# Performance work log

Hardware: AMD Instinct MI355X
Metric: run time of the kernel (lower is better)

Reference implementation:

```python
import jax, jax.numpy as jnp
import numpy as np
from jax import lax

B, H, W, CIN = 16, 96, 320, 32
N_ACTIVE = 200000
COUT = 256
FC_IN = (H // 8) * (W // 8) * 128  # 12*40*128 = 61440


def _conv(x, w, b):
    # stride-2, pad-1, 3x3 conv in NCHW / OIHW layout
    y = lax.conv_general_dilated(x, w, (2, 2), [(1, 1), (1, 1)],
                                 dimension_numbers=('NCHW', 'OIHW', 'NCHW'))
    return y + b[None, :, None, None]


def _maxpool3(x):
    # 3x3 maxpool, stride 1, pad 1 (NCHW)
    return lax.reduce_window(x, -jnp.inf, lax.max,
                             (1, 1, 3, 3), (1, 1, 1, 1),
                             [(0, 0), (0, 0), (1, 1), (1, 1)])


def setup_inputs() -> dict:
    key = jax.random.key(0)
    ks = jax.random.split(key, 12)
    input_feat = jax.random.normal(ks[0], (B, H, W, CIN), dtype=jnp.float32)
    cb = jax.random.randint(ks[1], (N_ACTIVE, 1), 0, B)
    cy = jax.random.randint(ks[2], (N_ACTIVE, 1), 0, H)
    cx = jax.random.randint(ks[3], (N_ACTIVE, 1), 0, W)
    spconv_coords = jnp.concatenate([cb, cy, cx], axis=1).astype(jnp.int32)
    w1 = jax.random.normal(ks[4], (32, CIN, 3, 3), dtype=jnp.float32) * (1.0 / np.sqrt(CIN * 9))
    b1 = jax.random.normal(ks[5], (32,), dtype=jnp.float32) * 0.01
    w2 = jax.random.normal(ks[6], (64, 32, 3, 3), dtype=jnp.float32) * (1.0 / np.sqrt(32 * 9))
    b2 = jax.random.normal(ks[7], (64,), dtype=jnp.float32) * 0.01
    w3 = jax.random.normal(ks[8], (128, 64, 3, 3), dtype=jnp.float32) * (1.0 / np.sqrt(64 * 9))
    b3 = jax.random.normal(ks[9], (128,), dtype=jnp.float32) * 0.01
    fc_w = jax.random.normal(ks[10], (COUT, FC_IN), dtype=jnp.float32) * (1.0 / np.sqrt(FC_IN))
    fc_b = jax.random.normal(ks[11], (COUT,), dtype=jnp.float32) * 0.01
    return {"input_feat": input_feat, "spconv_coords": spconv_coords,
            "w1": w1, "b1": b1, "w2": w2, "b2": b2, "w3": w3, "b3": b3,
            "fc_w": fc_w, "fc_b": fc_b}


def reference(input_feat, spconv_coords, w1, b1, w2, b2, w3, b3, fc_w, fc_b):
    bi = spconv_coords[:, 0]
    yi = spconv_coords[:, 1]
    xi = spconv_coords[:, 2]
    # gather active-site features, then scatter into a dense NHWC grid
    feats = input_feat[bi, yi, xi]                       # [N, CIN]
    dense = jnp.zeros_like(input_feat).at[bi, yi, xi].set(feats)
    x = dense.transpose(0, 3, 1, 2)                      # [B, CIN, H, W]
    x = jax.nn.relu(_maxpool3(_conv(x, w1, b1)))         # [B, 32, H/2, W/2]
    x = jax.nn.relu(_maxpool3(_conv(x, w2, b2)))         # [B, 64, H/4, W/4]
    x = jax.nn.relu(_maxpool3(_conv(x, w3, b3)))         # [B, 128, H/8, W/8]
    x = x.reshape(x.shape[0], -1)                        # [B, FC_IN]
    return jax.nn.relu(x @ fc_w.T + fc_b)                # [B, COUT]
```

## Files before the change

### kernel.cpp

```cpp
#include <hip/hip_runtime.h>

#define NB 16
#define NH 96
#define NW 320
#define NCIN 32

typedef __attribute__((ext_vector_type(8))) short short8;
typedef __attribute__((ext_vector_type(4))) float f32x4;

__device__ inline unsigned short f2bf(float f) {
    union { float f; unsigned int u; } v; v.f = f;
    unsigned int r = v.u + 0x7FFF + ((v.u >> 16) & 1);
    return (unsigned short)(r >> 16);
}

__global__ __launch_bounds__(256) void setup_all(const float* __restrict__ w1,
                                                 const float* __restrict__ w2,
                                                 const float* __restrict__ w3,
                                                 unsigned short* __restrict__ f1,
                                                 unsigned short* __restrict__ f2,
                                                 unsigned short* __restrict__ f3,
                                                 const int* __restrict__ coords,
                                                 const float* __restrict__ input,
                                                 unsigned short* __restrict__ inBf,
                                                 int n) {
    if (blockIdx.x < 396) {
        int i = blockIdx.x * 256 + threadIdx.x;
        if (i < 9216) {
            int j = i & 7, lane = (i >> 3) & 63, nt = (i >> 9) & 1, tap = i >> 10;
            int ic = ((lane >> 4) * 8) + j, oc = nt * 16 + (lane & 15);
            f1[i] = f2bf(w1[(oc * 32 + ic) * 9 + tap]);
        } else if (i < 27648) {
            int v = i - 9216;
            int j = v & 7, lane = (v >> 3) & 63, nt = (v >> 9) & 3, tap = v >> 11;
            int ic = ((lane >> 4) * 8) + j, oc = nt * 16 + (lane & 15);
            f2[v] = f2bf(w2[(oc * 32 + ic) * 9 + tap]);
        } else if (i < 101376) {
            int v = i - 27648;
            int j = v & 7, lane = (v >> 3) & 63, nt = (v >> 9) & 7, kk = v >> 12;
            int tap = kk >> 1, ks = kk & 1;
            int ic = ks * 32 + ((lane >> 4) * 8) + j, oc = nt * 16 + (lane & 15);
            f3[v] = f2bf(w3[(oc * 64 + ic) * 9 + tap]);
        }
    } else {
        int i = (blockIdx.x - 396) * 256 + threadIdx.x;
        if (i >= n * 4) return;
        int ci = i >> 2, q = i & 3;
        int b = coords[ci * 3 + 0], y = coords[ci * 3 + 1], x = coords[ci * 3 + 2];
        long base = ((long)((b * NH + y) * NW + x)) * NCIN + q * 8;
        const float4* src = (const float4*)(input + base);
        float4 v0 = src[0], v1 = src[1];
        union { short8 s8; unsigned short us[8]; } o;
        o.us[0] = f2bf(v0.x); o.us[1] = f2bf(v0.y); o.us[2] = f2bf(v0.z); o.us[3] = f2bf(v0.w);
        o.us[4] = f2bf(v1.x); o.us[5] = f2bf(v1.y); o.us[6] = f2bf(v1.z); o.us[7] = f2bf(v1.w);
        *(short8*)(inBf + base) = o.s8;
    }
}

template<int IC, int OC, int NL, int IH, int IW, int OH, int OW>
__global__ __launch_bounds__(256) void conv_mfma(
    const unsigned short* __restrict__ inPtr,
    const unsigned short* __restrict__ wfrag,
    const float* __restrict__ bias,
    float* __restrict__ out)
{
    constexpr int KS = IC / 32;
    constexpr int NT = OC / 16;
    constexpr int NG = NT / NL;
    constexpr int NSTRIPS = NB * OH * OW / 16;

    const int wid  = (blockIdx.x * 256 + threadIdx.x) >> 6;
    const int lane = threadIdx.x & 63;
    const int ntb  = (wid % NG) * NL;
    const int s    = wid / NG;
    if (s >= NSTRIPS) return;
    const int quad = lane >> 4;
    const int lm   = lane & 15;

    const int p0 = s * 16;
    const int posA = p0 + lm;
    const int b  = posA / (OH * OW);
    const int rr = posA % (OH * OW);
    const int oy = rr / OW, ox = rr % OW;
    const int iy0 = oy * 2 - 1, ix0 = ox * 2 - 1;

    int cell[9];
    bool okb[9];
    #pragma unroll
    for (int t9 = 0; t9 < 9; t9++) {
        const int iy = iy0 + t9 / 3;
        const int ix = ix0 + t9 % 3;
        const bool ok = (iy >= 0) && (iy < IH) && (ix >= 0) && (ix < IW);
        cell[t9] = ok ? ((b * IH + iy) * IW + ix) : 0;
        okb[t9] = ok;
    }

    short8 zero8;
    #pragma unroll
    for (int j = 0; j < 8; j++) zero8[j] = 0;

    f32x4 acc[NL][2];
    #pragma unroll
    for (int nl = 0; nl < NL; nl++)
        #pragma unroll
        for (int pp = 0; pp < 2; pp++)
            acc[nl][pp] = (f32x4){0.f, 0.f, 0.f, 0.f};

    #pragma unroll 1
    for (int ks = 0; ks < KS; ks++) {
        short8 av[9];
        #pragma unroll
        for (int t9 = 0; t9 < 9; t9++) {
            short8 v = *(const short8*)(inPtr + (long)cell[t9] * IC + ks * 32 + quad * 8);
            av[t9] = okb[t9] ? v : zero8;
        }
        #pragma unroll
        for (int nl = 0; nl < NL; nl++) {
            #pragma unroll
            for (int t9 = 0; t9 < 9; t9++) {
                short8 bf = *(const short8*)(wfrag + (((t9 * KS + ks) * NT + ntb + nl) * 64 + lane) * 8);
                if (t9 & 1) acc[nl][1] = __builtin_amdgcn_mfma_f32_16x16x32_bf16(av[t9], bf, acc[nl][1], 0, 0, 0);
                else        acc[nl][0] = __builtin_amdgcn_mfma_f32_16x16x32_bf16(av[t9], bf, acc[nl][0], 0, 0, 0);
            }
        }
    }

    const long rowBase = (long)p0 + quad * 4;
    #pragma unroll
    for (int nl = 0; nl < NL; nl++) {
        const int oc = (ntb + nl) * 16 + lm;
        const float bv = bias[oc];
        #pragma unroll
        for (int reg = 0; reg < 4; reg++)
            out[(rowBase + reg) * OC + oc] = acc[nl][0][reg] + acc[nl][1][reg] + bv;
    }
}

template<int C, int HH, int WW, bool BF16OUT>
__global__ __launch_bounds__(256) void maxpool3_relu(const float* __restrict__ in, void* __restrict__ outv) {
    constexpr int C4 = C / 4;
    int i = blockIdx.x * blockDim.x + threadIdx.x;
    if (i >= NB * HH * WW * C4) return;
    int c = i % C4;
    int x = (i / C4) % WW;
    int y = (i / (C4 * WW)) % HH;
    int b = i / (C4 * WW * HH);
    float4 m = make_float4(-3.0e38f, -3.0e38f, -3.0e38f, -3.0e38f);
    #pragma unroll
    for (int dy = -1; dy <= 1; dy++) {
        int yy = y + dy;
        if (yy < 0 || yy >= HH) continue;
        #pragma unroll
        for (int dx = -1; dx <= 1; dx++) {
            int xx = x + dx;
            if (xx < 0 || xx >= WW) continue;
            float4 v = ((const float4*)in)[((b * HH + yy) * WW + xx) * C4 + c];
            m.x = fmaxf(m.x, v.x);
            m.y = fmaxf(m.y, v.y);
            m.z = fmaxf(m.z, v.z);
            m.w = fmaxf(m.w, v.w);
        }
    }
    m.x = fmaxf(m.x, 0.f);
    m.y = fmaxf(m.y, 0.f);
    m.z = fmaxf(m.z, 0.f);
    m.w = fmaxf(m.w, 0.f);
    if (BF16OUT) {
        ushort4 o;
        o.x = f2bf(m.x); o.y = f2bf(m.y); o.z = f2bf(m.z); o.w = f2bf(m.w);
        ((ushort4*)outv)[i] = o;
    } else {
        ((float4*)outv)[i] = m;
    }
}

__global__ __launch_bounds__(256) void transpose_fc(const float* __restrict__ in, float* __restrict__ xT) {
    __shared__ float tile_s[32 * 16 * 17];
    const int pt = blockIdx.x % 30;
    const int ct = blockIdx.x / 30;
    const int pos0 = pt * 16, c0 = ct * 32;
    const int t = threadIdx.x;
    {
        const int b = t / 16, pl = t % 16;
        const float4* src = (const float4*)(in + ((long)(b * 480 + pos0 + pl)) * 128 + c0);
        #pragma unroll
        for (int q = 0; q < 8; q++) {
            float4 v = src[q];
            tile_s[((4 * q + 0) * 16 + pl) * 17 + b] = v.x;
            tile_s[((4 * q + 1) * 16 + pl) * 17 + b] = v.y;
            tile_s[((4 * q + 2) * 16 + pl) * 17 + b] = v.z;
            tile_s[((4 * q + 3) * 16 + pl) * 17 + b] = v.w;
        }
    }
    __syncthreads();
    {
        const int w = t / 64, l = t % 64;
        const int pl2 = l / 4, b4 = l % 4;
        #pragma unroll
        for (int i = 0; i < 8; i++) {
            int cl = w + 4 * i;
            const float* ls = &tile_s[(cl * 16 + pl2) * 17 + 4 * b4];
            float4 v = make_float4(ls[0], ls[1], ls[2], ls[3]);
            *(float4*)(xT + ((long)(c0 + cl) * 480 + pos0 + pl2) * 16 + 4 * b4) = v;
        }
    }
}

__global__ __launch_bounds__(256) void fc_stage1(const float* __restrict__ xT,
                                                 const float* __restrict__ fw,
                                                 float* __restrict__ partial)
{
    __shared__ float red[32 * 257];
    const int tile  = blockIdx.x / 15;
    const int chunk = blockIdx.x % 15;
    const int t = threadIdx.x;
    const int K = 61440, KC = 4096;

    float acc[4][16];
    #pragma unroll
    for (int o = 0; o < 4; o++)
        #pragma unroll
        for (int bb = 0; bb < 16; bb++) acc[o][bb] = 0.f;

    const int k0 = chunk * KC;
    #pragma unroll 2
    for (int k = k0 + t; k < k0 + KC; k += 256) {
        const float4* xp = (const float4*)(xT + (long)k * 16);
        float4 x0 = xp[0], x1 = xp[1], x2 = xp[2], x3 = xp[3];
        #pragma unroll
        for (int o = 0; o < 4; o++) {
            float w = fw[(long)(tile * 4 + o) * K + k];
            acc[o][0]  = fmaf(w, x0.x, acc[o][0]);
            acc[o][1]  = fmaf(w, x0.y, acc[o][1]);
            acc[o][2]  = fmaf(w, x0.z, acc[o][2]);
            acc[o][3]  = fmaf(w, x0.w, acc[o][3]);
            acc[o][4]  = fmaf(w, x1.x, acc[o][4]);
            acc[o][5]  = fmaf(w, x1.y, acc[o][5]);
            acc[o][6]  = fmaf(w, x1.z, acc[o][6]);
            acc[o][7]  = fmaf(w, x1.w, acc[o][7]);
            acc[o][8]  = fmaf(w, x2.x, acc[o][8]);
            acc[o][9]  = fmaf(w, x2.y, acc[o][9]);
            acc[o][10] = fmaf(w, x2.z, acc[o][10]);
            acc[o][11] = fmaf(w, x2.w, acc[o][11]);
            acc[o][12] = fmaf(w, x3.x, acc[o][12]);
            acc[o][13] = fmaf(w, x3.y, acc[o][13]);
            acc[o][14] = fmaf(w, x3.z, acc[o][14]);
            acc[o][15] = fmaf(w, x3.w, acc[o][15]);
        }
    }

    #pragma unroll
    for (int oo = 0; oo < 2; oo++)
        #pragma unroll
        for (int bb = 0; bb < 16; bb++)
            red[(oo * 16 + bb) * 257 + t] = acc[oo][bb];
    __syncthreads();
    if (t < 32) {
        float s = 0.f;
        for (int i = 0; i < 256; i++) s += red[t * 257 + i];
        partial[((long)chunk * 256 + tile * 4 + (t / 16)) * 16 + (t % 16)] = s;
    }
    __syncthreads();
    #pragma unroll
    for (int oo = 0; oo < 2; oo++)
        #pragma unroll
        for (int bb = 0; bb < 16; bb++)
            red[(oo * 16 + bb) * 257 + t] = acc[2 + oo][bb];
    __syncthreads();
    if (t < 32) {
        float s = 0.f;
        for (int i = 0; i < 256; i++) s += red[t * 257 + i];
        partial[((long)chunk * 256 + tile * 4 + 2 + (t / 16)) * 16 + (t % 16)] = s;
    }
}

__global__ __launch_bounds__(256) void fc_reduce(const float* __restrict__ partial,
                                                 const float* __restrict__ fcb,
                                                 float* __restrict__ out)
{
    int i = blockIdx.x * blockDim.x + threadIdx.x;
    if (i >= 4096) return;
    int oc = i / 16, b = i % 16;
    float s = fcb[oc];
    #pragma unroll
    for (int c = 0; c < 15; c++) s += partial[(c * 256 + oc) * 16 + b];
    out[b * 256 + oc] = fmaxf(s, 0.f);
}

extern "C" void kernel_launch(void* const* d_in, const int* in_sizes, int n_in,
                              void* d_out, int out_size, void* d_ws, size_t ws_size,
                              hipStream_t stream) {
    const float* input  = (const float*)d_in[0];
    const int*   coords = (const int*)d_in[1];
    const float* w1 = (const float*)d_in[2];
    const float* b1 = (const float*)d_in[3];
    const float* w2 = (const float*)d_in[4];
    const float* b2 = (const float*)d_in[5];
    const float* w3 = (const float*)d_in[6];
    const float* b3 = (const float*)d_in[7];
    const float* fcw = (const float*)d_in[8];
    const float* fcb = (const float*)d_in[9];
    float* outp = (float*)d_out;

    const int n_active = in_sizes[1] / 3;

    char* ws = (char*)d_ws;
    unsigned short* wf1 = (unsigned short*)ws;
    unsigned short* wf2 = wf1 + 9216;
    unsigned short* wf3 = wf2 + 18432;
    unsigned short* inBf = (unsigned short*)(ws + 204800);
    char* regA = ws + 204800 + 31457280;
    char* regB = regA + 15728640;
    float* partial = (float*)(regB + 7864320);

    float*          conv1o  = (float*)regA;
    unsigned short* pool1bf = (unsigned short*)regB;
    float*          conv2o  = (float*)regA;
    unsigned short* pool2bf = (unsigned short*)regB;
    float*          conv3o  = (float*)regA;
    float*          pool3f  = (float*)regB;
    float*          xT      = (float*)regA;

    hipMemsetAsync(inBf, 0, 31457280, stream);
    const int scatterBlocks = (n_active * 4 + 255) / 256;
    setup_all<<<396 + scatterBlocks, 256, 0, stream>>>(w1, w2, w3, wf1, wf2, wf3,
                                                       coords, input, inBf, n_active);

    conv_mfma<32, 32, 2, 96, 320, 48, 160>
        <<<1920, 256, 0, stream>>>(inBf, wf1, b1, conv1o);
    maxpool3_relu<32, 48, 160, true><<<3840, 256, 0, stream>>>(conv1o, pool1bf);

    conv_mfma<32, 64, 2, 48, 160, 24, 80>
        <<<960, 256, 0, stream>>>(pool1bf, wf2, b2, conv2o);
    maxpool3_relu<64, 24, 80, true><<<1920, 256, 0, stream>>>(conv2o, pool2bf);

    conv_mfma<64, 128, 2, 24, 80, 12, 40>
        <<<480, 256, 0, stream>>>(pool2bf, wf3, b3, conv3o);
    maxpool3_relu<128, 12, 40, false><<<960, 256, 0, stream>>>(conv3o, pool3f);

    transpose_fc<<<120, 256, 0, stream>>>(pool3f, xT);
    fc_stage1<<<960, 256, 0, stream>>>(xT, fcw, partial);
    fc_reduce<<<16, 256, 0, stream>>>(partial, fcb, outp);
}
```

Before: 246.8 us.

## Compute FC layer with bf16 MFMA and split-K across 240 chunks

Replaces the scalar FMA FC kernel with a wave-level bf16 MFMA kernel: each wave handles 16 output channels over a 256-wide K chunk, converting fp32 weights to bf16 on the fly. The transpose kernel now writes activations as bf16 in batch-major [B, K] layout to feed the MFMA A operand. The final reduction now sums 240 partials per output instead of 15. The aim is to cut FMA issue cost and the shared-memory reduction, at the cost of bf16 precision in the FC and more partial-sum traffic.

```diff
diff --git a/kernel.cpp b/kernel.cpp
--- a/kernel.cpp
+++ b/kernel.cpp
@@ -174,7 +174,8 @@
     }
 }
 
-__global__ __launch_bounds__(256) void transpose_fc(const float* __restrict__ in, float* __restrict__ xT) {
+__global__ __launch_bounds__(256) void transpose_fc(const float* __restrict__ in,
+                                                    unsigned short* __restrict__ xb) {
     __shared__ float tile_s[32 * 16 * 17];
     const int pt = blockIdx.x % 30;
     const int ct = blockIdx.x / 30;
@@ -194,83 +195,61 @@
     }
     __syncthreads();
     {
-        const int w = t / 64, l = t % 64;
-        const int pl2 = l / 4, b4 = l % 4;
-        #pragma unroll
-        for (int i = 0; i < 8; i++) {
-            int cl = w + 4 * i;
-            const float* ls = &tile_s[(cl * 16 + pl2) * 17 + 4 * b4];
-            float4 v = make_float4(ls[0], ls[1], ls[2], ls[3]);
-            *(float4*)(xT + ((long)(c0 + cl) * 480 + pos0 + pl2) * 16 + 4 * b4) = v;
-        }
-    }
-}
-
-__global__ __launch_bounds__(256) void fc_stage1(const float* __restrict__ xT,
-                                                 const float* __restrict__ fw,
-                                                 float* __restrict__ partial)
+        #pragma unroll
+        for (int r = 0; r < 2; r++) {
+            int seg = t * 2 + r;
+            int b = seg / 32, cl = seg % 32;
+            union { short8 s8; unsigned short us[8]; } o0, o1;
+            #pragma unroll
+            for (int pl = 0; pl < 8; pl++)
+                o0.us[pl] = f2bf(tile_s[(cl * 16 + pl) * 17 + b]);
+            #pragma unroll
+            for (int pl = 0; pl < 8; pl++)
+                o1.us[pl] = f2bf(tile_s[(cl * 16 + 8 + pl) * 17 + b]);
+            unsigned short* dst = xb + (long)b * 61440 + (c0 + cl) * 480 + pos0;
+            *(short8*)dst = o0.s8;
+            *(short8*)(dst + 8) = o1.s8;
+        }
+    }
+}
+
+__global__ __launch_bounds__(256) void fc_mfma(const unsigned short* __restrict__ xb,
+                                               const float* __restrict__ fw,
+                                               float* __restrict__ partial)
 {
-    __shared__ float red[32 * 257];
-    const int tile  = blockIdx.x / 15;
-    const int chunk = blockIdx.x % 15;
-    const int t = threadIdx.x;
-    const int K = 61440, KC = 4096;
-
-    float acc[4][16];
-    #pragma unroll
-    for (int o = 0; o < 4; o++)
-        #pragma unroll
-        for (int bb = 0; bb < 16; bb++) acc[o][bb] = 0.f;
-
-    const int k0 = chunk * KC;
-    #pragma unroll 2
-    for (int k = k0 + t; k < k0 + KC; k += 256) {
-        const float4* xp = (const float4*)(xT + (long)k * 16);
-        float4 x0 = xp[0], x1 = xp[1], x2 = xp[2], x3 = xp[3];
-        #pragma unroll
-        for (int o = 0; o < 4; o++) {
-            float w = fw[(long)(tile * 4 + o) * K + k];
-            acc[o][0]  = fmaf(w, x0.x, acc[o][0]);
-            acc[o][1]  = fmaf(w, x0.y, acc[o][1]);
-            acc[o][2]  = fmaf(w, x0.z, acc[o][2]);
-            acc[o][3]  = fmaf(w, x0.w, acc[o][3]);
-            acc[o][4]  = fmaf(w, x1.x, acc[o][4]);
-            acc[o][5]  = fmaf(w, x1.y, acc[o][5]);
-            acc[o][6]  = fmaf(w, x1.z, acc[o][6]);
-            acc[o][7]  = fmaf(w, x1.w, acc[o][7]);
-            acc[o][8]  = fmaf(w, x2.x, acc[o][8]);
-            acc[o][9]  = fmaf(w, x2.y, acc[o][9]);
-            acc[o][10] = fmaf(w, x2.z, acc[o][10]);
-            acc[o][11] = fmaf(w, x2.w, acc[o][11]);
-            acc[o][12] = fmaf(w, x3.x, acc[o][12]);
-            acc[o][13] = fmaf(w, x3.y, acc[o][13]);
-            acc[o][14] = fmaf(w, x3.z, acc[o][14]);
-            acc[o][15] = fmaf(w, x3.w, acc[o][15]);
-        }
-    }
-
-    #pragma unroll
-    for (int oo = 0; oo < 2; oo++)
-        #pragma unroll
-        for (int bb = 0; bb < 16; bb++)
-            red[(oo * 16 + bb) * 257 + t] = acc[oo][bb];
-    __syncthreads();
-    if (t < 32) {
-        float s = 0.f;
-        for (int i = 0; i < 256; i++) s += red[t * 257 + i];
-        partial[((long)chunk * 256 + tile * 4 + (t / 16)) * 16 + (t % 16)] = s;
-    }
-    __syncthreads();
-    #pragma unroll
-    for (int oo = 0; oo < 2; oo++)
-        #pragma unroll
-        for (int bb = 0; bb < 16; bb++)
-            red[(oo * 16 + bb) * 257 + t] = acc[2 + oo][bb];
-    __syncthreads();
-    if (t < 32) {
-        float s = 0.f;
-        for (int i = 0; i < 256; i++) s += red[t * 257 + i];
-        partial[((long)chunk * 256 + tile * 4 + 2 + (t / 16)) * 16 + (t % 16)] = s;
+    const int wid  = (blockIdx.x * 256 + threadIdx.x) >> 6;
+    const int lane = threadIdx.x & 63;
+    const int tile  = wid / 240;
+    const int chunk = wid % 240;
+    const int quad = lane >> 4;
+    const int lm   = lane & 15;
+    const int K = 61440;
+    const int k0 = chunk * 256;
+
+    const unsigned short* xrow = xb + (long)lm * K;
+    const float* wrow = fw + (long)(tile * 16 + lm) * K;
+
+    f32x4 acc0 = {0.f, 0.f, 0.f, 0.f};
+    f32x4 acc1 = {0.f, 0.f, 0.f, 0.f};
+    #pragma unroll
+    for (int st = 0; st < 8; st++) {
+        const int k = k0 + st * 32 + quad * 8;
+        short8 a = *(const short8*)(xrow + k);
+        float4 w0 = *(const float4*)(wrow + k);
+        float4 w1 = *(const float4*)(wrow + k + 4);
+        union { short8 s8; unsigned short us[8]; } bb;
+        bb.us[0] = f2bf(w0.x); bb.us[1] = f2bf(w0.y);
+        bb.us[2] = f2bf(w0.z); bb.us[3] = f2bf(w0.w);
+        bb.us[4] = f2bf(w1.x); bb.us[5] = f2bf(w1.y);
+        bb.us[6] = f2bf(w1.z); bb.us[7] = f2bf(w1.w);
+        if (st & 1) acc1 = __builtin_amdgcn_mfma_f32_16x16x32_bf16(a, bb.s8, acc1, 0, 0, 0);
+        else        acc0 = __builtin_amdgcn_mfma_f32_16x16x32_bf16(a, bb.s8, acc0, 0, 0, 0);
+    }
+
+    #pragma unroll
+    for (int reg = 0; reg < 4; reg++) {
+        float v = acc0[reg] + acc1[reg];
+        partial[((long)chunk * 256 + tile * 16 + lm) * 16 + quad * 4 + reg] = v;
     }
 }
 
@@ -282,8 +261,8 @@
     if (i >= 4096) return;
     int oc = i / 16, b = i % 16;
     float s = fcb[oc];
-    #pragma unroll
-    for (int c = 0; c < 15; c++) s += partial[(c * 256 + oc) * 16 + b];
+    #pragma unroll 4
+    for (int c = 0; c < 240; c++) s += partial[((long)c * 256 + oc) * 16 + b];
     out[b * 256 + oc] = fmaxf(s, 0.f);
 }
 
@@ -319,7 +298,7 @@
     unsigned short* pool2bf = (unsigned short*)regB;
     float*          conv3o  = (float*)regA;
     float*          pool3f  = (float*)regB;
-    float*          xT      = (float*)regA;
+    unsigned short* xb      = (unsigned short*)regA;
 
     hipMemsetAsync(inBf, 0, 31457280, stream);
     const int scatterBlocks = (n_active * 4 + 255) / 256;
@@ -338,7 +317,7 @@
         <<<480, 256, 0, stream>>>(pool2bf, wf3, b3, conv3o);
     maxpool3_relu<128, 12, 40, false><<<960, 256, 0, stream>>>(conv3o, pool3f);
 
-    transpose_fc<<<120, 256, 0, stream>>>(pool3f, xT);
-    fc_stage1<<<960, 256, 0, stream>>>(xT, fcw, partial);
+    transpose_fc<<<120, 256, 0, stream>>>(pool3f, xb);
+    fc_mfma<<<960, 256, 0, stream>>>(xb, fcw, partial);
     fc_reduce<<<16, 256, 0, stream>>>(partial, fcb, outp);
 }
```

Result: slower. 254.7 us (+3.2%).
